# Optimization experiments

Measured on AMD Instinct MI355X. Metric: run time of the kernel, lower is better.

## Reference

```python
import jax, jax.numpy as jnp
import numpy as np

B = 8192   # batch
S = 115    # state dim (fixed by slice layout)
E = 3072   # retrieval embed dim
C = 128    # compressed context dim
A = 23     # action dim
NE = 4096  # number of hyperedge keys
K = 10     # top-k retrieval
TAU = 1.0  # gumbel temperature
EPS = 1e-5 # layernorm eps


def _ln(x, g, b):
    m = x.mean(-1, keepdims=True)
    v = x.var(-1, keepdims=True)
    return (x - m) * jax.lax.rsqrt(v + EPS) * g + b


def _actor(ctx, extra, w1, b1, g1, be1, w2, b2, g2, be2, w3, b3):
    x = jnp.concatenate([ctx, extra], -1)
    x = jax.nn.relu(_ln(x @ w1 + b1, g1, be1))
    x = jax.nn.relu(_ln(x @ w2 + b2, g2, be2))
    return x @ w3 + b3


def setup_inputs() -> dict:
    key = jax.random.key(0)
    ks = iter(jax.random.split(key, 80))

    def W(shape):
        return jax.random.normal(next(ks), shape, jnp.float32) * (1.0 / float(np.sqrt(shape[0])))

    inp = {}
    inp["state"] = jax.random.normal(next(ks), (B, S), jnp.float32)
    u = jax.random.uniform(next(ks), (B, 4), jnp.float32, 1e-6, 1.0 - 1e-6)
    inp["gumbel_noise"] = -jnp.log(-jnp.log(u))  # standard Gumbel samples
    inp["keys"] = jax.random.normal(next(ks), (NE, E), jnp.float32)
    # state encoder 115 -> 512 -> 512 -> 3072 + LN
    inp["se_w1"] = W((S, 512)); inp["se_b1"] = jnp.zeros(512)
    inp["se_w2"] = W((512, 512)); inp["se_b2"] = jnp.zeros(512)
    inp["se_w3"] = W((512, E)); inp["se_b3"] = jnp.zeros(E)
    inp["se_g"] = jnp.ones(E); inp["se_beta"] = jnp.zeros(E)
    # context compressor 3072 -> 512 -> 128 + LN
    inp["cc_w1"] = W((E, 512)); inp["cc_b1"] = jnp.zeros(512)
    inp["cc_w2"] = W((512, C)); inp["cc_b2"] = jnp.zeros(C)
    inp["cc_g"] = jnp.ones(C); inp["cc_beta"] = jnp.zeros(C)
    # 4 actor experts, differing only in extra-slice width
    for p, e in [("a_pre", 50), ("a_scene", 20), ("a_effect", 10), ("a_rule", 15)]:
        inp[p + "_w1"] = W((C + e, C)); inp[p + "_b1"] = jnp.zeros(C)
        inp[p + "_g1"] = jnp.ones(C); inp[p + "_be1"] = jnp.zeros(C)
        inp[p + "_w2"] = W((C, C)); inp[p + "_b2"] = jnp.zeros(C)
        inp[p + "_g2"] = jnp.ones(C); inp[p + "_be2"] = jnp.zeros(C)
        inp[p + "_w3"] = W((C, A)) * 0.01; inp[p + "_b3"] = jnp.zeros(A)  # orthogonal gain=0.01 approx
    # gumbel router 115 -> 64 -> 64 -> 4
    inp["r_w1"] = W((S, 64)); inp["r_b1"] = jnp.zeros(64)
    inp["r_w2"] = W((64, 64)); inp["r_b2"] = jnp.zeros(64)
    inp["r_w3"] = W((64, 4)); inp["r_b3"] = jnp.zeros(4)
    # critic 115 -> 256 -> 256 -> 1
    inp["c_w1"] = W((S, 256)); inp["c_b1"] = jnp.zeros(256)
    inp["c_w2"] = W((256, 256)); inp["c_b2"] = jnp.zeros(256)
    inp["c_w3"] = W((256, 1)); inp["c_b3"] = jnp.zeros(1)
    return inp


def reference(state, gumbel_noise, keys, se_w1, se_b1, se_w2, se_b2, se_w3, se_b3, se_g, se_beta, cc_w1, cc_b1, cc_w2, cc_b2, cc_g, cc_beta, a_pre_w1, a_pre_b1, a_pre_g1, a_pre_be1, a_pre_w2, a_pre_b2, a_pre_g2, a_pre_be2, a_pre_w3, a_pre_b3, a_scene_w1, a_scene_b1, a_scene_g1, a_scene_be1, a_scene_w2, a_scene_b2, a_scene_g2, a_scene_be2, a_scene_w3, a_scene_b3, a_effect_w1, a_effect_b1, a_effect_g1, a_effect_be1, a_effect_w2, a_effect_b2, a_effect_g2, a_effect_be2, a_effect_w3, a_effect_b3, a_rule_w1, a_rule_b1, a_rule_g1, a_rule_be1, a_rule_w2, a_rule_b2, a_rule_g2, a_rule_be2, a_rule_w3, a_rule_b3, r_w1, r_b1, r_w2, r_b2, r_w3, r_b3, c_w1, c_b1, c_w2, c_b2, c_w3, c_b3):
    # 1) state -> query (StateEncoder)
    q = jax.nn.relu(state @ se_w1 + se_b1)
    q = jax.nn.relu(q @ se_w2 + se_b2)
    q = _ln(q @ se_w3 + se_b3, se_g, se_beta)  # (B, E)
    # 2) top-k hard retrieval from hypergraph memory (cosine sim)
    qn = q * jax.lax.rsqrt(jnp.sum(q * q, -1, keepdims=True) + 1e-12)
    kn = keys * jax.lax.rsqrt(jnp.sum(keys * keys, -1, keepdims=True) + 1e-12)
    scores = qn @ kn.T                          # (B, NE)
    _, idx = jax.lax.top_k(scores, K)           # (B, K)
    context = jnp.take(keys, idx, axis=0).mean(1)  # (B, E) mean-pool top-k raw embeddings
    # 3) compress to shared knowledge
    h = jax.nn.relu(context @ cc_w1 + cc_b1)
    shared = _ln(h @ cc_w2 + cc_b2, cc_g, cc_beta)  # (B, C)
    # 4) state slices + 4 actor experts
    belief = state[:, :50]
    location = state[:, 20:40]
    hp = state[:, 40:50]
    inv = state[:, 45:60]
    lp = _actor(shared, belief, a_pre_w1, a_pre_b1, a_pre_g1, a_pre_be1, a_pre_w2, a_pre_b2, a_pre_g2, a_pre_be2, a_pre_w3, a_pre_b3)
    ls = _actor(shared, location, a_scene_w1, a_scene_b1, a_scene_g1, a_scene_be1, a_scene_w2, a_scene_b2, a_scene_g2, a_scene_be2, a_scene_w3, a_scene_b3)
    le = _actor(shared, hp, a_effect_w1, a_effect_b1, a_effect_g1, a_effect_be1, a_effect_w2, a_effect_b2, a_effect_g2, a_effect_be2, a_effect_w3, a_effect_b3)
    lr = _actor(shared, inv, a_rule_w1, a_rule_b1, a_rule_g1, a_rule_be1, a_rule_w2, a_rule_b2, a_rule_g2, a_rule_be2, a_rule_w3, a_rule_b3)
    # 5) gumbel-softmax hard router (straight-through)
    rh = jax.nn.relu(state @ r_w1 + r_b1)
    rh = jax.nn.relu(rh @ r_w2 + r_b2)
    rl = jnp.clip(rh @ r_w3 + r_b3, -20.0, 20.0)
    y_soft = jax.nn.softmax((rl + gumbel_noise) / TAU, -1)
    y_hard = jax.nn.one_hot(jnp.argmax(y_soft, -1), 4, dtype=y_soft.dtype)
    alpha = y_soft + jax.lax.stop_gradient(y_hard - y_soft)  # (B, 4)
    # 6) combine expert logits
    all_l = jnp.stack([lp, ls, le, lr], 1)      # (B, 4, A)
    logits = jnp.einsum('bk,bka->ba', alpha, all_l)
    # critic value
    v = jax.nn.relu(state @ c_w1 + c_b1)
    v = jax.nn.relu(v @ c_w2 + c_b2)
    value = v @ c_w3 + c_b3                      # (B, 1)
    return (logits, alpha, value)
```

## Files before the change

### kernel.cpp

```cpp
#include <hip/hip_runtime.h>

constexpr int Bz = 8192;
constexpr int Sz = 115;
constexpr int Ez = 3072;
constexpr int NEz = 4096;

typedef __attribute__((ext_vector_type(8))) short short8;
typedef __attribute__((ext_vector_type(4))) float floatx4;
typedef unsigned short ushort_t;
typedef unsigned int uint_t;

__device__ __forceinline__ ushort_t f2bf(float f) {
  uint_t u = __float_as_uint(f);
  uint_t r = (u + 0x7FFFu + ((u >> 16) & 1u)) >> 16;
  return (ushort_t)r;
}
__device__ __forceinline__ float bf2f(ushort_t b) {
  uint_t u = ((uint_t)b) << 16;
  return __uint_as_float(u);
}
__device__ __forceinline__ ushort_t f2key(float v) {
  _Float16 h = (_Float16)v;
  ushort_t b = __builtin_bit_cast(ushort_t, h);
  return b ^ ((b & 0x8000u) ? 0xFFFFu : 0x8000u);
}
__device__ __forceinline__ uint_t umax_(uint_t a, uint_t b) { return a > b ? a : b; }

__device__ __forceinline__ void gload16(const ushort_t* g, ushort_t* l) {
  __builtin_amdgcn_global_load_lds(
      (__attribute__((address_space(1))) const void*)g,
      (__attribute__((address_space(3))) void*)l, 16, 0, 0);
}

template<bool RELU, bool BIAS>
__global__ __launch_bounds__(256)
void gemm128(const float* __restrict__ A, const float* __restrict__ Bm,
             const float* __restrict__ bias, float* __restrict__ C,
             int N, int Kd)
{
  __shared__ float As[16][132];
  __shared__ float Bs[16][132];
  const int t  = threadIdx.x;
  const int tx = t & 15, ty = t >> 4;
  const int row0 = blockIdx.y * 128;
  const int col0 = blockIdx.x * 128;
  const int ar = t >> 2, ac = (t & 3) * 4;
  const int bk = t >> 5, bc = (t & 31) * 4;
  const bool a4 = (Kd & 3) == 0;

  float acc[8][8];
#pragma unroll
  for (int i = 0; i < 8; ++i)
#pragma unroll
    for (int j = 0; j < 8; ++j) acc[i][j] = 0.f;

  for (int k0 = 0; k0 < Kd; k0 += 16) {
    const bool fullA = (k0 + 16 <= Kd) && a4;
    {
      const float* ap = A + (size_t)(row0 + ar) * Kd + k0 + ac;
      if (fullA) {
        float4 v0 = *(const float4*)ap;
        float4 v1 = *(const float4*)(ap + (size_t)64 * Kd);
        As[ac + 0][ar] = v0.x; As[ac + 1][ar] = v0.y;
        As[ac + 2][ar] = v0.z; As[ac + 3][ar] = v0.w;
        As[ac + 0][ar + 64] = v1.x; As[ac + 1][ar + 64] = v1.y;
        As[ac + 2][ar + 64] = v1.z; As[ac + 3][ar + 64] = v1.w;
      } else {
#pragma unroll
        for (int e = 0; e < 4; ++e) {
          const int k = k0 + ac + e;
          float v0 = 0.f, v1 = 0.f;
          if (k < Kd) { v0 = ap[e]; v1 = ap[e + (size_t)64 * Kd]; }
          As[ac + e][ar] = v0; As[ac + e][ar + 64] = v1;
        }
      }
    }
    {
      const float* bp = Bm + (size_t)(k0 + bk) * N + col0 + bc;
      if (k0 + 16 <= Kd) {
        *(float4*)&Bs[bk][bc]     = *(const float4*)bp;
        *(float4*)&Bs[bk + 8][bc] = *(const float4*)(bp + (size_t)8 * N);
      } else {
        float4 z; z.x = z.y = z.z = z.w = 0.f;
        *(float4*)&Bs[bk][bc]     = (k0 + bk     < Kd) ? *(const float4*)bp : z;
        *(float4*)&Bs[bk + 8][bc] = (k0 + bk + 8 < Kd) ? *(const float4*)(bp + (size_t)8 * N) : z;
      }
    }
    __syncthreads();
#pragma unroll
    for (int kk = 0; kk < 16; ++kk) {
      float a[8], b[8];
      *(float4*)&a[0] = *(const float4*)&As[kk][ty * 4];
      *(float4*)&a[4] = *(const float4*)&As[kk][64 + ty * 4];
      *(float4*)&b[0] = *(const float4*)&Bs[kk][tx * 4];
      *(float4*)&b[4] = *(const float4*)&Bs[kk][64 + tx * 4];
#pragma unroll
      for (int i = 0; i < 8; ++i)
#pragma unroll
        for (int j = 0; j < 8; ++j)
          acc[i][j] = fmaf(a[i], b[j], acc[i][j]);
    }
    __syncthreads();
  }

  float bv[8];
#pragma unroll
  for (int j = 0; j < 8; ++j) bv[j] = 0.f;
  if (BIAS) {
    *(float4*)&bv[0] = *(const float4*)&bias[col0 + tx * 4];
    *(float4*)&bv[4] = *(const float4*)&bias[col0 + 64 + tx * 4];
  }
#pragma unroll
  for (int i = 0; i < 8; ++i) {
    const int r = row0 + ((i < 4) ? (ty * 4 + i) : (64 + ty * 4 + i - 4));
    float o[8];
#pragma unroll
    for (int j = 0; j < 8; ++j) {
      o[j] = acc[i][j] + bv[j];
      if (RELU) o[j] = fmaxf(o[j], 0.f);
    }
    *(float4*)&C[(size_t)r * N + col0 + tx * 4]      = *(float4*)&o[0];
    *(float4*)&C[(size_t)r * N + col0 + 64 + tx * 4] = *(float4*)&o[4];
  }
}

template<int EPI>
__global__ __launch_bounds__(256)
void mfma_bt(const ushort_t* __restrict__ A, const ushort_t* __restrict__ B,
             const float* __restrict__ bias, void* __restrict__ Cout,
             int N, int Kd)
{
  __shared__ ushort_t Al[128 * 32];
  __shared__ ushort_t Bl[128 * 32];
  const int t = threadIdx.x;
  const int wid = t >> 6, lane = t & 63;
  const int wr = wid >> 1, wc = wid & 1;
  const int row0 = blockIdx.y * 128;
  const int col0 = blockIdx.x * 128;
  const int srow = lane >> 2;
  const int scol = (lane & 3) * 8;

  const ushort_t* ga0 = A + (size_t)(row0 + wid * 16 + srow) * Kd + scol;
  const ushort_t* ga1 = A + (size_t)(row0 + (wid + 4) * 16 + srow) * Kd + scol;
  const ushort_t* gb0 = B + (size_t)(col0 + wid * 16 + srow) * Kd + scol;
  const ushort_t* gb1 = B + (size_t)(col0 + (wid + 4) * 16 + srow) * Kd + scol;
  ushort_t* la0 = &Al[(wid * 16) * 32];
  ushort_t* la1 = &Al[((wid + 4) * 16) * 32];
  ushort_t* lb0 = &Bl[(wid * 16) * 32];
  ushort_t* lb1 = &Bl[((wid + 4) * 16) * 32];

  const int mr = lane & 15, qd = lane >> 4;

  floatx4 acc[4][4];
#pragma unroll
  for (int i = 0; i < 4; ++i)
#pragma unroll
    for (int j = 0; j < 4; ++j) acc[i][j] = (floatx4){0.f, 0.f, 0.f, 0.f};

  for (int kb = 0; kb < Kd; kb += 32) {
    gload16(ga0 + kb, la0);
    gload16(ga1 + kb, la1);
    gload16(gb0 + kb, lb0);
    gload16(gb1 + kb, lb1);
    __syncthreads();
    short8 aF[4], bF[4];
#pragma unroll
    for (int i = 0; i < 4; ++i)
      aF[i] = *(const short8*)&Al[(wr * 64 + i * 16 + mr) * 32 + qd * 8];
#pragma unroll
    for (int j = 0; j < 4; ++j)
      bF[j] = *(const short8*)&Bl[(wc * 64 + j * 16 + mr) * 32 + qd * 8];
#pragma unroll
    for (int i = 0; i < 4; ++i)
#pragma unroll
      for (int j = 0; j < 4; ++j)
        acc[i][j] = __builtin_amdgcn_mfma_f32_16x16x32_bf16(aF[i], bF[j], acc[i][j], 0, 0, 0);
    __syncthreads();
  }

#pragma unroll
  for (int i = 0; i < 4; ++i) {
#pragma unroll
    for (int j = 0; j < 4; ++j) {
      const int col = col0 + wc * 64 + j * 16 + mr;
#pragma unroll
      for (int r = 0; r < 4; ++r) {
        const int row = row0 + wr * 64 + i * 16 + qd * 4 + r;
        if (EPI == 0) {
          ((ushort_t*)Cout)[(size_t)row * N + col] = f2key(acc[i][j][r]);
        } else {
          float v = acc[i][j][r] + bias[col];
          ((float*)Cout)[(size_t)row * N + col] = fmaxf(v, 0.f);
        }
      }
    }
  }
}

__global__ __launch_bounds__(256)
void mfma3_bt(const ushort_t* __restrict__ Ah, const ushort_t* __restrict__ Alo,
              const ushort_t* __restrict__ Bh, const ushort_t* __restrict__ Blo,
              const float* __restrict__ bias, float* __restrict__ Cout,
              int N, int Kd)
{
  __shared__ ushort_t AhL[128 * 32];
  __shared__ ushort_t AlL[128 * 32];
  __shared__ ushort_t BhL[128 * 32];
  __shared__ ushort_t BlL[128 * 32];
  const int t = threadIdx.x;
  const int wid = t >> 6, lane = t & 63;
  const int wr = wid >> 1, wc = wid & 1;
  const int row0 = blockIdx.y * 128;
  const int col0 = blockIdx.x * 128;
  const int srow = lane >> 2;
  const int scol = (lane & 3) * 8;

  const size_t aoff0 = (size_t)(row0 + wid * 16 + srow) * Kd + scol;
  const size_t aoff1 = (size_t)(row0 + (wid + 4) * 16 + srow) * Kd + scol;
  const size_t boff0 = (size_t)(col0 + wid * 16 + srow) * Kd + scol;
  const size_t boff1 = (size_t)(col0 + (wid + 4) * 16 + srow) * Kd + scol;
  const int l0 = (wid * 16) * 32;
  const int l1 = ((wid + 4) * 16) * 32;

  const int mr = lane & 15, qd = lane >> 4;

  floatx4 acc[4][4];
#pragma unroll
  for (int i = 0; i < 4; ++i)
#pragma unroll
    for (int j = 0; j < 4; ++j) acc[i][j] = (floatx4){0.f, 0.f, 0.f, 0.f};

  for (int kb = 0; kb < Kd; kb += 32) {
    gload16(Ah + aoff0 + kb, &AhL[l0]);
    gload16(Ah + aoff1 + kb, &AhL[l1]);
    gload16(Alo + aoff0 + kb, &AlL[l0]);
    gload16(Alo + aoff1 + kb, &AlL[l1]);
    gload16(Bh + boff0 + kb, &BhL[l0]);
    gload16(Bh + boff1 + kb, &BhL[l1]);
    gload16(Blo + boff0 + kb, &BlL[l0]);
    gload16(Blo + boff1 + kb, &BlL[l1]);
    __syncthreads();
    short8 ahF[4], alF[4], bhF[4], blF[4];
#pragma unroll
    for (int i = 0; i < 4; ++i) {
      const int o = (wr * 64 + i * 16 + mr) * 32 + qd * 8;
      ahF[i] = *(const short8*)&AhL[o];
      alF[i] = *(const short8*)&AlL[o];
    }
#pragma unroll
    for (int j = 0; j < 4; ++j) {
      const int o = (wc * 64 + j * 16 + mr) * 32 + qd * 8;
      bhF[j] = *(const short8*)&BhL[o];
      blF[j] = *(const short8*)&BlL[o];
    }
#pragma unroll
    for (int i = 0; i < 4; ++i)
#pragma unroll
      for (int j = 0; j < 4; ++j) {
        acc[i][j] = __builtin_amdgcn_mfma_f32_16x16x32_bf16(alF[i], bhF[j], acc[i][j], 0, 0, 0);
        acc[i][j] = __builtin_amdgcn_mfma_f32_16x16x32_bf16(ahF[i], blF[j], acc[i][j], 0, 0, 0);
        acc[i][j] = __builtin_amdgcn_mfma_f32_16x16x32_bf16(ahF[i], bhF[j], acc[i][j], 0, 0, 0);
      }
    __syncthreads();
  }

#pragma unroll
  for (int i = 0; i < 4; ++i) {
#pragma unroll
    for (int j = 0; j < 4; ++j) {
      const int col = col0 + wc * 64 + j * 16 + mr;
#pragma unroll
      for (int r = 0; r < 4; ++r) {
        const int row = row0 + wr * 64 + i * 16 + qd * 4 + r;
        Cout[(size_t)row * N + col] = acc[i][j][r] + bias[col];
      }
    }
  }
}

__global__ __launch_bounds__(256)
void gemm_scores(const float* __restrict__ A, const float* __restrict__ Bm,
                 const float* __restrict__ rk, ushort_t* __restrict__ S)
{
  __shared__ float As[16][132];
  __shared__ float Bs[16][132];
  const int t  = threadIdx.x;
  const int tx = t & 15, ty = t >> 4;
  const int row0 = blockIdx.y * 128;
  const int col0 = blockIdx.x * 128;
  const int ar = t >> 2, ac = (t & 3) * 4;
  const int Kd = Ez;

  float acc[8][8];
#pragma unroll
  for (int i = 0; i < 8; ++i)
#pragma unroll
    for (int j = 0; j < 8; ++j) acc[i][j] = 0.f;

  for (int k0 = 0; k0 < Kd; k0 += 16) {
    {
      const float* ap = A + (size_t)(row0 + ar) * Kd + k0 + ac;
      float4 v0 = *(const float4*)ap;
      float4 v1 = *(const float4*)(ap + (size_t)64 * Kd);
      As[ac + 0][ar] = v0.x; As[ac + 1][ar] = v0.y;
      As[ac + 2][ar] = v0.z; As[ac + 3][ar] = v0.w;
      As[ac + 0][ar + 64] = v1.x; As[ac + 1][ar + 64] = v1.y;
      As[ac + 2][ar + 64] = v1.z; As[ac + 3][ar + 64] = v1.w;
    }
    {
      const float* bp = Bm + (size_t)(col0 + ar) * Kd + k0 + ac;
      float4 v0 = *(const float4*)bp;
      float4 v1 = *(const float4*)(bp + (size_t)64 * Kd);
      Bs[ac + 0][ar] = v0.x; Bs[ac + 1][ar] = v0.y;
      Bs[ac + 2][ar] = v0.z; Bs[ac + 3][ar] = v0.w;
      Bs[ac + 0][ar + 64] = v1.x; Bs[ac + 1][ar + 64] = v1.y;
      Bs[ac + 2][ar + 64] = v1.z; Bs[ac + 3][ar + 64] = v1.w;
    }
    __syncthreads();
#pragma unroll
    for (int kk = 0; kk < 16; ++kk) {
      float a[8], b[8];
      *(float4*)&a[0] = *(const float4*)&As[kk][ty * 4];
      *(float4*)&a[4] = *(const float4*)&As[kk][64 + ty * 4];
      *(float4*)&b[0] = *(const float4*)&Bs[kk][tx * 4];
      *(float4*)&b[4] = *(const float4*)&Bs[kk][64 + tx * 4];
#pragma unroll
      for (int i = 0; i < 8; ++i)
#pragma unroll
        for (int j = 0; j < 8; ++j)
          acc[i][j] = fmaf(a[i], b[j], acc[i][j]);
    }
    __syncthreads();
  }

  float rk0[8];
  *(float4*)&rk0[0] = *(const float4*)&rk[col0 + tx * 4];
  *(float4*)&rk0[4] = *(const float4*)&rk[col0 + 64 + tx * 4];
#pragma unroll
  for (int i = 0; i < 8; ++i) {
    const int r = row0 + ((i < 4) ? (ty * 4 + i) : (64 + ty * 4 + i - 4));
    ushort4 h0, h1;
    h0.x = f2key(acc[i][0] * rk0[0]); h0.y = f2key(acc[i][1] * rk0[1]);
    h0.z = f2key(acc[i][2] * rk0[2]); h0.w = f2key(acc[i][3] * rk0[3]);
    h1.x = f2key(acc[i][4] * rk0[4]); h1.y = f2key(acc[i][5] * rk0[5]);
    h1.z = f2key(acc[i][6] * rk0[6]); h1.w = f2key(acc[i][7] * rk0[7]);
    *(ushort4*)&S[(size_t)r * NEz + col0 + tx * 4]      = h0;
    *(ushort4*)&S[(size_t)r * NEz + col0 + 64 + tx * 4] = h1;
  }
}

struct LN4 {
  const float* W[4]; const float* b[4]; const float* g[4]; const float* be[4];
  int eoff[4]; int elen[4];
};

template<bool RELU, bool HASEXT>
__global__ __launch_bounds__(256)
void gemm_ln4(const float* __restrict__ A1base, size_t a1stride, int K1,
              const float* __restrict__ A2, LN4 p,
              float* __restrict__ outbase, size_t ostride)
{
  __shared__ float As[32][68];
  __shared__ float Bs[32][132];
  __shared__ float rsum[64][17];
  __shared__ float rsq[64][17];
  __shared__ float stm[64], str[64];
  const int a = blockIdx.y;
  const float* A1 = A1base + (size_t)a * a1stride;
  float* out = outbase + (size_t)a * ostride;
  const float* W = p.W[a];
  const float* bias = p.b[a];
  const float* g = p.g[a];
  const float* be = p.be[a];
  const int eoff = HASEXT ? p.eoff[a] : 0;
  const int K2 = HASEXT ? p.elen[a] : 0;

  const int t = threadIdx.x;
  const int tx = t & 15, ty = t >> 4;
  const int row0 = blockIdx.x * 64;
  const int Kt = K1 + K2;
  const int ar = t >> 2, ac = (t & 3) * 8;
  const int bk = t >> 3, bc = (t & 7) * 16;

  float acc[4][8];
#pragma unroll
  for (int i = 0; i < 4; ++i)
#pragma unroll
    for (int j = 0; j < 8; ++j) acc[i][j] = 0.f;

  for (int k0 = 0; k0 < Kt; k0 += 32) {
    const int grow = row0 + ar;
#pragma unroll
    for (int e = 0; e < 8; ++e) {
      const int k = k0 + ac + e;
      float v = 0.f;
      if (k < K1)      v = A1[(size_t)grow * K1 + k];
      else if (k < Kt) v = A2[(size_t)grow * 115 + eoff + (k - K1)];
      As[ac + e][ar] = v;
    }
    {
      const int k = k0 + bk;
#pragma unroll
      for (int qd = 0; qd < 4; ++qd) {
        float4 z; z.x = z.y = z.z = z.w = 0.f;
        *(float4*)&Bs[bk][bc + 4 * qd] =
            (k < Kt) ? *(const float4*)&W[(size_t)k * 128 + bc + 4 * qd] : z;
      }
    }
    __syncthreads();
#pragma unroll
    for (int kk = 0; kk < 32; ++kk) {
      float av[4], bv2[8];
      *(float4*)&av[0]  = *(const float4*)&As[kk][ty * 4];
      *(float4*)&bv2[0] = *(const float4*)&Bs[kk][tx * 4];
      *(float4*)&bv2[4] = *(const float4*)&Bs[kk][64 + tx * 4];
#pragma unroll
      for (int i = 0; i < 4; ++i)
#pragma unroll
        for (int j = 0; j < 8; ++j)
          acc[i][j] = fmaf(av[i], bv2[j], acc[i][j]);
    }
    __syncthreads();
  }

  float bv[8];
  *(float4*)&bv[0] = *(const float4*)&bias[tx * 4];
  *(float4*)&bv[4] = *(const float4*)&bias[64 + tx * 4];
#pragma unroll
  for (int i = 0; i < 4; ++i) {
    float s = 0.f, q = 0.f;
#pragma unroll
    for (int j = 0; j < 8; ++j) {
      acc[i][j] += bv[j];
      s += acc[i][j];
      q += acc[i][j] * acc[i][j];
    }
    rsum[ty * 4 + i][tx] = s;
    rsq[ty * 4 + i][tx]  = q;
  }
  __syncthreads();
  if (t < 64) {
    float s = 0.f, q = 0.f;
#pragma unroll
    for (int x = 0; x < 16; ++x) { s += rsum[t][x]; q += rsq[t][x]; }
    const float m = s * (1.f / 128.f);
    const float v = q * (1.f / 128.f) - m * m;
    stm[t] = m;
    str[t] = rsqrtf(v + 1e-5f);
  }
  __syncthreads();
#pragma unroll
  for (int i = 0; i < 4; ++i) {
    const int r = ty * 4 + i;
    const float m = stm[r], rs = str[r];
    float o[8];
#pragma unroll
    for (int j = 0; j < 8; ++j) {
      const int col = (j < 4) ? (tx * 4 + j) : (64 + tx * 4 + (j - 4));
      float y = (acc[i][j] - m) * rs * g[col] + be[col];
      if (RELU) y = fmaxf(y, 0.f);
      o[j] = y;
    }
    *(float4*)&out[(size_t)(row0 + r) * 128 + tx * 4]      = *(float4*)&o[0];
    *(float4*)&out[(size_t)(row0 + r) * 128 + 64 + tx * 4] = *(float4*)&o[4];
  }
}

__device__ __forceinline__ float blockSum256(float v, float* sh)
{
#pragma unroll
  for (int d = 32; d; d >>= 1) v += __shfl_down(v, d, 64);
  __syncthreads();
  if ((threadIdx.x & 63) == 0) sh[threadIdx.x >> 6] = v;
  __syncthreads();
  return sh[0] + sh[1] + sh[2] + sh[3];
}

template<bool CVT>
__global__ __launch_bounds__(256)
void ln_l2_q(float* __restrict__ q, const float* __restrict__ g,
             const float* __restrict__ be, ushort_t* __restrict__ qb)
{
  __shared__ float sh[4];
  const int row = blockIdx.x, t = threadIdx.x;
  float* qr = q + (size_t)row * Ez;
  float x[12];
#pragma unroll
  for (int i = 0; i < 12; ++i) x[i] = qr[t + (i << 8)];
  float s = 0.f;
#pragma unroll
  for (int i = 0; i < 12; ++i) s += x[i];
  const float m = blockSum256(s, sh) * (1.f / (float)Ez);
  float vs = 0.f;
#pragma unroll
  for (int i = 0; i < 12; ++i) { const float d = x[i] - m; vs += d * d; }
  const float v = blockSum256(vs, sh) * (1.f / (float)Ez);
  const float rs = rsqrtf(v + 1e-5f);
  float y[12]; float qs = 0.f;
#pragma unroll
  for (int i = 0; i < 12; ++i) {
    const int c = t + (i << 8);
    const float yy = (x[i] - m) * rs * g[c] + be[c];
    y[i] = yy; qs += yy * yy;
  }
  const float tot = blockSum256(qs, sh);
  const float s2 = rsqrtf(tot + 1e-12f);
#pragma unroll
  for (int i = 0; i < 12; ++i) {
    const int c = t + (i << 8);
    const float yn = y[i] * s2;
    qr[c] = yn;
    if (CVT) qb[(size_t)row * Ez + c] = f2bf(yn);
  }
}

__global__ __launch_bounds__(256)
void keynorm(const float* __restrict__ keys, float* __restrict__ rk)
{
  __shared__ float sh[4];
  const int row = blockIdx.x, t = threadIdx.x;
  const float* xr = keys + (size_t)row * Ez;
  float qs = 0.f;
#pragma unroll
  for (int i = 0; i < 12; ++i) { const float x = xr[t + (i << 8)]; qs += x * x; }
  const float tot = blockSum256(qs, sh);
  if (t == 0) rk[row] = rsqrtf(tot + 1e-12f);
}

__global__ __launch_bounds__(256)
void keys_norm_cvt(const float* __restrict__ keys, float* __restrict__ rk,
                   ushort_t* __restrict__ knb)
{
  __shared__ float sh[4];
  const int row = blockIdx.x, t = threadIdx.x;
  const float* xr = keys + (size_t)row * Ez;
  float x[12]; float qs = 0.f;
#pragma unroll
  for (int i = 0; i < 12; ++i) { x[i] = xr[t + (i << 8)]; qs += x[i] * x[i]; }
  const float tot = blockSum256(qs, sh);
  const float s = rsqrtf(tot + 1e-12f);
  if (t == 0) rk[row] = s;
#pragma unroll
  for (int i = 0; i < 12; ++i)
    knb[(size_t)row * Ez + t + (i << 8)] = f2bf(x[i] * s);
}

__global__ __launch_bounds__(256)
void split_bf(const float* __restrict__ in, ushort_t* __restrict__ oh,
              ushort_t* __restrict__ ol)
{
  const size_t i = ((size_t)blockIdx.x * 256 + threadIdx.x) * 4;
  float4 v = *(const float4*)(in + i);
  ushort4 h, l;
  h.x = f2bf(v.x); l.x = f2bf(v.x - bf2f(h.x));
  h.y = f2bf(v.y); l.y = f2bf(v.y - bf2f(h.y));
  h.z = f2bf(v.z); l.z = f2bf(v.z - bf2f(h.z));
  h.w = f2bf(v.w); l.w = f2bf(v.w - bf2f(h.w));
  *(ushort4*)(oh + i) = h;
  *(ushort4*)(ol + i) = l;
}

__global__ __launch_bounds__(256)
void w3_transpose_split(const float* __restrict__ w,
                        ushort_t* __restrict__ hT, ushort_t* __restrict__ lT)
{
  __shared__ float tile[64][65];
  const int k0 = blockIdx.x * 64;
  const int n0 = blockIdx.y * 64;
  const int t = threadIdx.x;
  const int c = t & 63, r4 = t >> 6;
#pragma unroll
  for (int rr = 0; rr < 16; ++rr) {
    const int r = rr * 4 + r4;
    tile[r][c] = w[(size_t)(k0 + r) * 3072 + n0 + c];
  }
  __syncthreads();
#pragma unroll
  for (int rr = 0; rr < 16; ++rr) {
    const int n = rr * 4 + r4;
    const float a = tile[c][n];
    const ushort_t h = f2bf(a);
    hT[(size_t)(n0 + n) * 512 + k0 + c] = h;
    lT[(size_t)(n0 + n) * 512 + k0 + c] = f2bf(a - bf2f(h));
  }
}

__global__ __launch_bounds__(256)
void cvt_w1t(const float* __restrict__ w, ushort_t* __restrict__ out)
{
  const int idx = blockIdx.x * 256 + threadIdx.x;
  const int k = idx >> 9, n = idx & 511;
  out[(size_t)n * Ez + k] = f2bf(w[idx]);
}

__global__ __launch_bounds__(256)
void topk16(const ushort_t* __restrict__ S, int* __restrict__ outIdx)
{
  __shared__ uint_t cand[64];
  const int row = blockIdx.x, t = threadIdx.x;
  const int w = t >> 6, lane = t & 63;
  const ushort_t* sr = S + (size_t)row * NEz + (w << 10);
  uint_t p[16];
#pragma unroll
  for (int j = 0; j < 16; ++j) {
    const int c = (j << 6) + lane;
    const uint_t key = sr[c];
    const int gc = (w << 10) + c;
    p[j] = (key << 12) | (uint_t)(4095 - gc);
  }
  for (int it = 0; it < 16; ++it) {
    uint_t m = p[0];
#pragma unroll
    for (int j = 1; j < 16; ++j) m = umax_(m, p[j]);
#pragma unroll
    for (int d = 1; d < 64; d <<= 1)
      m = umax_(m, (uint_t)__shfl_xor((int)m, d, 64));
    if (lane == it) cand[(w << 4) + it] = m;
#pragma unroll
    for (int j = 0; j < 16; ++j) p[j] = (p[j] == m) ? 0u : p[j];
  }
  __syncthreads();
  if (t < 64) {
    uint_t mine = cand[t];
    for (int it = 0; it < 16; ++it) {
      uint_t m = mine;
#pragma unroll
      for (int d = 1; d < 64; d <<= 1)
        m = umax_(m, (uint_t)__shfl_xor((int)m, d, 64));
      if (t == it) outIdx[(size_t)row * 16 + it] = 4095 - (int)(m & 0xFFFu);
      mine = (mine == m) ? 0u : mine;
    }
  }
}

template<bool BFOUT>
__global__ __launch_bounds__(256)
void rescore_gather(const float* __restrict__ qn, const float* __restrict__ keys,
                    const float* __restrict__ rk, const int* __restrict__ cand,
                    void* __restrict__ ctxOut)
{
  __shared__ float qs[Ez];
  __shared__ double sv[16];
  __shared__ int si[16];
  __shared__ int sel10[10];
  const int row = blockIdx.x, t = threadIdx.x;
  const int w = t >> 6, lane = t & 63;

  {
    const float* qr = qn + (size_t)row * Ez;
#pragma unroll
    for (int i = 0; i < 3; ++i) {
      const int c = (t << 2) + (i << 10);
      *(float4*)&qs[c] = *(const float4*)&qr[c];
    }
  }
  __syncthreads();

#pragma unroll
  for (int cc = 0; cc < 4; ++cc) {
    const int slot = w * 4 + cc;
    const int id = cand[(size_t)row * 16 + slot];
    const float* kr = keys + (size_t)id * Ez;
    double s = 0.0;
#pragma unroll
    for (int it = 0; it < 12; ++it) {
      const int c = (lane << 2) + (it << 8);
      float4 k4 = *(const float4*)&kr[c];
      float4 q4 = *(const float4*)&qs[c];
      s += (double)q4.x * (double)k4.x;
      s += (double)q4.y * (double)k4.y;
      s += (double)q4.z * (double)k4.z;
      s += (double)q4.w * (double)k4.w;
    }
#pragma unroll
    for (int d = 32; d; d >>= 1) s += __shfl_down(s, d, 64);
    if (lane == 0) { sv[slot] = s * (double)rk[id]; si[slot] = id; }
  }
  __syncthreads();

  if (t == 0) {
    for (int it = 0; it < 10; ++it) {
      int bj = 0; double bvv = sv[0]; int bi = si[0];
      for (int j = 1; j < 16; ++j) {
        const double v = sv[j]; const int i2 = si[j];
        if (v > bvv || (v == bvv && i2 < bi)) { bj = j; bvv = v; bi = i2; }
      }
      sel10[it] = bi;
      sv[bj] = -1e300;
    }
  }
  __syncthreads();

  int id[10];
#pragma unroll
  for (int j = 0; j < 10; ++j) id[j] = sel10[j];

#pragma unroll
  for (int i = 0; i < 3; ++i) {
    const int c = (t << 2) + (i << 10);
    float4 a = {0.f, 0.f, 0.f, 0.f};
#pragma unroll
    for (int j = 0; j < 10; ++j) {
      float4 v = *(const float4*)&keys[(size_t)id[j] * Ez + c];
      a.x += v.x; a.y += v.y; a.z += v.z; a.w += v.w;
    }
    if (BFOUT) {
      ushort4 o;
      o.x = f2bf(a.x * 0.1f); o.y = f2bf(a.y * 0.1f);
      o.z = f2bf(a.z * 0.1f); o.w = f2bf(a.w * 0.1f);
      *(ushort4*)&((ushort_t*)ctxOut)[(size_t)row * Ez + c] = o;
    } else {
      float4 o;
      o.x = a.x * 0.1f; o.y = a.y * 0.1f; o.z = a.z * 0.1f; o.w = a.w * 0.1f;
      *(float4*)&((float*)ctxOut)[(size_t)row * Ez + c] = o;
    }
  }
}

__global__ __launch_bounds__(256)
void router_kernel(const float* __restrict__ state, const float* __restrict__ gn,
                   const float* __restrict__ w1, const float* __restrict__ b1,
                   const float* __restrict__ w2, const float* __restrict__ b2,
                   const float* __restrict__ w3, const float* __restrict__ b3,
                   float* __restrict__ outAlpha)
{
  const int row = blockIdx.x * 256 + threadIdx.x;
  const float* sr = state + (size_t)row * Sz;
  float h1[64];
#pragma unroll
  for (int j = 0; j < 64; ++j) h1[j] = b1[j];
  for (int k = 0; k < Sz; ++k) {
    const float a = sr[k];
    const float* wr = w1 + (size_t)k * 64;
#pragma unroll
    for (int j = 0; j < 64; ++j) h1[j] = fmaf(a, wr[j], h1[j]);
  }
#pragma unroll
  for (int j = 0; j < 64; ++j) h1[j] = fmaxf(h1[j], 0.f);
  float h2[64];
#pragma unroll
  for (int j = 0; j < 64; ++j) h2[j] = b2[j];
#pragma unroll
  for (int k = 0; k < 64; ++k) {
    const float a = h1[k];
    const float* wr = w2 + (size_t)k * 64;
#pragma unroll
    for (int j = 0; j < 64; ++j) h2[j] = fmaf(a, wr[j], h2[j]);
  }
#pragma unroll
  for (int j = 0; j < 64; ++j) h2[j] = fmaxf(h2[j], 0.f);
  float z[4];
#pragma unroll
  for (int a = 0; a < 4; ++a) {
    float s = b3[a];
#pragma unroll
    for (int k = 0; k < 64; ++k) s = fmaf(h2[k], w3[k * 4 + a], s);
    s = fminf(fmaxf(s, -20.f), 20.f);
    z[a] = s + gn[(size_t)row * 4 + a];
  }
  float mz = z[0];
#pragma unroll
  for (int a = 1; a < 4; ++a) mz = fmaxf(mz, z[a]);
  float e[4]; float se = 0.f;
#pragma unroll
  for (int a = 0; a < 4; ++a) { e[a] = expf(z[a] - mz); se += e[a]; }
  const float inv = 1.f / se;
  float y[4];
#pragma unroll
  for (int a = 0; a < 4; ++a) y[a] = e[a] * inv;
  int am = 0;
#pragma unroll
  for (int a = 1; a < 4; ++a) if (y[a] > y[am]) am = a;
#pragma unroll
  for (int a = 0; a < 4; ++a) {
    const float hard = (a == am) ? 1.f : 0.f;
    outAlpha[(size_t)row * 4 + a] = y[a] + (hard - y[a]);
  }
}

__global__ __launch_bounds__(256)
void critic_head(const float* __restrict__ c2, const float* __restrict__ w3,
                 const float* __restrict__ b3, float* __restrict__ outv)
{
  const int row = blockIdx.x * 256 + threadIdx.x;
  const float* xr = c2 + (size_t)row * 256;
  float s = b3[0];
  for (int k = 0; k < 256; ++k) s = fmaf(xr[k], w3[k], s);
  outv[row] = s;
}

struct HeadP { const float* w3[4]; const float* b3[4]; };

__global__ __launch_bounds__(256)
void actor_head4(const float* __restrict__ x2g, HeadP p,
                 const float* __restrict__ alpha, float* __restrict__ outL)
{
  __shared__ float wsm[4][128 * 23];
  __shared__ float bs[4][23];
  const int t = threadIdx.x;
#pragma unroll
  for (int a = 0; a < 4; ++a) {
    for (int i = t; i < 128 * 23; i += 256) wsm[a][i] = p.w3[a][i];
    if (t < 23) bs[a][t] = p.b3[a][t];
  }
  __syncthreads();
  const int row = blockIdx.x * 64 + (t >> 2);
  const int cg = t & 3;
  float sum[6] = {0.f, 0.f, 0.f, 0.f, 0.f, 0.f};
#pragma unroll
  for (int a = 0; a < 4; ++a) {
    const float al = alpha[(size_t)row * 4 + a];
    const float* xr = x2g + (size_t)a * Bz * 128 + (size_t)row * 128;
    float acc[6] = {0.f, 0.f, 0.f, 0.f, 0.f, 0.f};
    for (int kk = 0; kk < 128; ++kk) {
      const float xa = xr[kk];
#pragma unroll
      for (int j = 0; j < 6; ++j) {
        const int col = cg + 4 * j;
        if (col < 23) acc[j] = fmaf(xa, wsm[a][kk * 23 + col], acc[j]);
      }
    }
#pragma unroll
    for (int j = 0; j < 6; ++j) {
      const int col = cg + 4 * j;
      if (col < 23) sum[j] += al * (acc[j] + bs[a][col]);
    }
  }
#pragma unroll
  for (int j = 0; j < 6; ++j) {
    const int col = cg + 4 * j;
    if (col < 23) outL[(size_t)row * 23 + col] = sum[j];
  }
}

extern "C" void kernel_launch(void* const* d_in, const int* in_sizes, int n_in,
                              void* d_out, int out_size, void* d_ws, size_t ws_size,
                              hipStream_t stream)
{
  const float* state  = (const float*)d_in[0];
  const float* gumbel = (const float*)d_in[1];
  const float* keys   = (const float*)d_in[2];
  const float* se_w1 = (const float*)d_in[3];
  const float* se_b1 = (const float*)d_in[4];
  const float* se_w2 = (const float*)d_in[5];
  const float* se_b2 = (const float*)d_in[6];
  const float* se_w3 = (const float*)d_in[7];
  const float* se_b3 = (const float*)d_in[8];
  const float* se_g  = (const float*)d_in[9];
  const float* se_be = (const float*)d_in[10];
  const float* cc_w1 = (const float*)d_in[11];
  const float* cc_b1 = (const float*)d_in[12];
  const float* cc_w2 = (const float*)d_in[13];
  const float* cc_b2 = (const float*)d_in[14];
  const float* cc_g  = (const float*)d_in[15];
  const float* cc_be = (const float*)d_in[16];
  const float* r_w1 = (const float*)d_in[57];
  const float* r_b1 = (const float*)d_in[58];
  const float* r_w2 = (const float*)d_in[59];
  const float* r_b2 = (const float*)d_in[60];
  const float* r_w3 = (const float*)d_in[61];
  const float* r_b3 = (const float*)d_in[62];
  const float* c_w1 = (const float*)d_in[63];
  const float* c_b1 = (const float*)d_in[64];
  const float* c_w2 = (const float*)d_in[65];
  const float* c_b2 = (const float*)d_in[66];
  const float* c_w3 = (const float*)d_in[67];
  const float* c_b3 = (const float*)d_in[68];

  float* wsf = (float*)d_ws;
  const size_t qF = (size_t)Bz * Ez;
  const size_t uF = (size_t)16777216;
  float* q = wsf;
  float* U = wsf + qF;
  float* sA  = U;
  float* sB  = U + 4194304;
  ushort_t* sBh  = (ushort_t*)(U + 8388608);
  ushort_t* sBl  = (ushort_t*)(U + 10485760);
  ushort_t* w3hT = (ushort_t*)(U + 12582912);
  ushort_t* w3lT = (ushort_t*)(U + 14155776);
  ushort_t* scoresU = (ushort_t*)U;
  float* shr = U;
  float* x1g = U + 1 * 1048576;
  float* x2g = U + 5 * 1048576;
  float* cch = U + 9 * 1048576;
  float* cr1 = U + 9 * 1048576;
  float* cr2 = U + 11 * 1048576;
  ushort_t* qbf  = (ushort_t*)(wsf + qF + uF);
  ushort_t* knbf = qbf + qF;
  ushort_t* w1T  = knbf + (size_t)NEz * Ez;
  const size_t bfHalves = qF + (size_t)NEz * Ez + (size_t)512 * Ez;
  const size_t baseBytes = (qF + uF) * sizeof(float);
  const size_t tailBytes = 4096 * 4 + (size_t)Bz * 16 * 4;
  const bool fast = ws_size >= baseBytes + bfHalves * 2 + tailBytes;
  float* tailF = (float*)((char*)d_ws + (fast ? baseBytes + bfHalves * 2 : baseBytes));
  float* rk  = tailF;
  int* cand  = (int*)(tailF + 4096);
  ushort_t* ctxb = (ushort_t*)q;

  float* outL = (float*)d_out;
  float* outA = outL + (size_t)Bz * 23;
  float* outV = outA + (size_t)Bz * 4;

  const dim3 blk(256);

  gemm128<true, true><<<dim3(4, 64), blk, 0, stream>>>(state, se_w1, se_b1, sA, 512, 115);
  gemm128<true, true><<<dim3(4, 64), blk, 0, stream>>>(sA,    se_w2, se_b2, sB, 512, 512);
  if (fast) {
    split_bf<<<dim3(4096), blk, 0, stream>>>(sB, sBh, sBl);
    w3_transpose_split<<<dim3(8, 48), blk, 0, stream>>>(se_w3, w3hT, w3lT);
    mfma3_bt<<<dim3(24, 64), blk, 0, stream>>>(sBh, sBl, w3hT, w3lT, se_b3, q, 3072, 512);
    ln_l2_q<true><<<dim3(Bz), blk, 0, stream>>>(q, se_g, se_be, qbf);
    keys_norm_cvt<<<dim3(NEz), blk, 0, stream>>>(keys, rk, knbf);
    cvt_w1t<<<dim3(6144), blk, 0, stream>>>(cc_w1, w1T);
    mfma_bt<0><<<dim3(32, 64), blk, 0, stream>>>(qbf, knbf, nullptr, scoresU, NEz, Ez);
  } else {
    gemm128<false, true><<<dim3(24, 64), blk, 0, stream>>>(sB, se_w3, se_b3, q, 3072, 512);
    ln_l2_q<false><<<dim3(Bz), blk, 0, stream>>>(q, se_g, se_be, nullptr);
    keynorm<<<dim3(NEz), blk, 0, stream>>>(keys, rk);
    gemm_scores<<<dim3(32, 64), blk, 0, stream>>>(q, keys, rk, scoresU);
  }

  topk16<<<dim3(Bz), blk, 0, stream>>>(scoresU, cand);

  if (fast) {
    rescore_gather<true><<<dim3(Bz), blk, 0, stream>>>(q, keys, rk, cand, ctxb);
    mfma_bt<1><<<dim3(4, 64), blk, 0, stream>>>(ctxb, w1T, cc_b1, cch, 512, Ez);
  } else {
    rescore_gather<false><<<dim3(Bz), blk, 0, stream>>>(q, keys, rk, cand, q);
    gemm128<true, true><<<dim3(4, 64), blk, 0, stream>>>(q, cc_w1, cc_b1, cch, 512, Ez);
  }
  {
    LN4 pcc = {};
    pcc.W[0] = cc_w2; pcc.b[0] = cc_b2; pcc.g[0] = cc_g; pcc.be[0] = cc_be;
    gemm_ln4<false, false><<<dim3(128, 1), blk, 0, stream>>>(cch, 0, 512, nullptr, pcc,
                                                             shr, 0);
  }

  gemm128<true, true><<<dim3(2, 64), blk, 0, stream>>>(state, c_w1, c_b1, cr1, 256, 115);
  gemm128<true, true><<<dim3(2, 64), blk, 0, stream>>>(cr1, c_w2, c_b2, cr2, 256, 256);
  critic_head<<<dim3(32), blk, 0, stream>>>(cr2, c_w3, c_b3, outV);

  router_kernel<<<dim3(32), blk, 0, stream>>>(state, gumbel, r_w1, r_b1, r_w2, r_b2,
                                              r_w3, r_b3, outA);

  {
    LN4 p1 = {}, p2 = {};
    HeadP ph = {};
    const int eoffs[4] = {0, 20, 40, 45};
    const int elens[4] = {50, 20, 10, 15};
    for (int a = 0; a < 4; ++a) {
      const int base = 17 + 10 * a;
      p1.W[a]  = (const float*)d_in[base + 0];
      p1.b[a]  = (const float*)d_in[base + 1];
      p1.g[a]  = (const float*)d_in[base + 2];
      p1.be[a] = (const float*)d_in[base + 3];
      p1.eoff[a] = eoffs[a]; p1.elen[a] = elens[a];
      p2.W[a]  = (const float*)d_in[base + 4];
      p2.b[a]  = (const float*)d_in[base + 5];
      p2.g[a]  = (const float*)d_in[base + 6];
      p2.be[a] = (const float*)d_in[base + 7];
      ph.w3[a] = (const float*)d_in[base + 8];
      ph.b3[a] = (const float*)d_in[base + 9];
    }
    gemm_ln4<true, true ><<<dim3(128, 4), blk, 0, stream>>>(shr, 0, 128, state, p1,
                                                            x1g, (size_t)Bz * 128);
    gemm_ln4<true, false><<<dim3(128, 4), blk, 0, stream>>>(x1g, (size_t)Bz * 128, 128,
                                                            nullptr, p2,
                                                            x2g, (size_t)Bz * 128);
    actor_head4<<<dim3(128), blk, 0, stream>>>(x2g, ph, outA, outL);
  }
}
```

Measured before the change: 1.437 ms.

## Batch critic GEMMs with encoder, fuse bf16 split, swizzle scores grid, vectorize topk

Critic MLP layers now share a launch with the state-encoder layers through a dual-problem GEMM kernel. The second of these also writes the hi/lo bf16 split in its epilogue, which removes the separate split kernel. The scores MFMA GEMM uses a 1D grid with a grouped tile swizzle for better L2 reuse, and cc_w1 is transposed through a shared-memory tile for coalesced access. topk16 loads 16 contiguous keys per lane with vector loads, and actor_head4 uses twice as many blocks with fewer columns per thread. Critic buffers are aliased onto q, which relies on q being dead at that point; critic and router now run before q is written.

```diff
diff --git a/kernel.cpp b/kernel.cpp
--- a/kernel.cpp
+++ b/kernel.cpp
@@ -124,6 +124,113 @@
   }
 }
 
+struct GPart {
+  const float* A; const float* Bm; const float* bias;
+  float* C; ushort_t* Ch; ushort_t* Cl;
+  int N; int Kd; int nbx;
+};
+
+__global__ __launch_bounds__(256)
+void gemm128_dual(GPart g0, GPart g1)
+{
+  __shared__ float As[16][132];
+  __shared__ float Bs[16][132];
+  const int t  = threadIdx.x;
+  const int tx = t & 15, ty = t >> 4;
+  const bool p0 = (int)blockIdx.x < g0.nbx;
+  GPart g = p0 ? g0 : g1;
+  const int bx = p0 ? blockIdx.x : (blockIdx.x - g0.nbx);
+  const int row0 = blockIdx.y * 128;
+  const int col0 = bx * 128;
+  const int Kd = g.Kd, N = g.N;
+  const int ar = t >> 2, ac = (t & 3) * 4;
+  const int bk = t >> 5, bc = (t & 31) * 4;
+  const bool a4 = (Kd & 3) == 0;
+
+  float acc[8][8];
+#pragma unroll
+  for (int i = 0; i < 8; ++i)
+#pragma unroll
+    for (int j = 0; j < 8; ++j) acc[i][j] = 0.f;
+
+  for (int k0 = 0; k0 < Kd; k0 += 16) {
+    const bool fullA = (k0 + 16 <= Kd) && a4;
+    {
+      const float* ap = g.A + (size_t)(row0 + ar) * Kd + k0 + ac;
+      if (fullA) {
+        float4 v0 = *(const float4*)ap;
+        float4 v1 = *(const float4*)(ap + (size_t)64 * Kd);
+        As[ac + 0][ar] = v0.x; As[ac + 1][ar] = v0.y;
+        As[ac + 2][ar] = v0.z; As[ac + 3][ar] = v0.w;
+        As[ac + 0][ar + 64] = v1.x; As[ac + 1][ar + 64] = v1.y;
+        As[ac + 2][ar + 64] = v1.z; As[ac + 3][ar + 64] = v1.w;
+      } else {
+#pragma unroll
+        for (int e = 0; e < 4; ++e) {
+          const int k = k0 + ac + e;
+          float v0 = 0.f, v1 = 0.f;
+          if (k < Kd) { v0 = ap[e]; v1 = ap[e + (size_t)64 * Kd]; }
+          As[ac + e][ar] = v0; As[ac + e][ar + 64] = v1;
+        }
+      }
+    }
+    {
+      const float* bp = g.Bm + (size_t)(k0 + bk) * N + col0 + bc;
+      if (k0 + 16 <= Kd) {
+        *(float4*)&Bs[bk][bc]     = *(const float4*)bp;
+        *(float4*)&Bs[bk + 8][bc] = *(const float4*)(bp + (size_t)8 * N);
+      } else {
+        float4 z; z.x = z.y = z.z = z.w = 0.f;
+        *(float4*)&Bs[bk][bc]     = (k0 + bk     < Kd) ? *(const float4*)bp : z;
+        *(float4*)&Bs[bk + 8][bc] = (k0 + bk + 8 < Kd) ? *(const float4*)(bp + (size_t)8 * N) : z;
+      }
+    }
+    __syncthreads();
+#pragma unroll
+    for (int kk = 0; kk < 16; ++kk) {
+      float a[8], b[8];
+      *(float4*)&a[0] = *(const float4*)&As[kk][ty * 4];
+      *(float4*)&a[4] = *(const float4*)&As[kk][64 + ty * 4];
+      *(float4*)&b[0] = *(const float4*)&Bs[kk][tx * 4];
+      *(float4*)&b[4] = *(const float4*)&Bs[kk][64 + tx * 4];
+#pragma unroll
+      for (int i = 0; i < 8; ++i)
+#pragma unroll
+        for (int j = 0; j < 8; ++j)
+          acc[i][j] = fmaf(a[i], b[j], acc[i][j]);
+    }
+    __syncthreads();
+  }
+
+  float bv[8];
+  *(float4*)&bv[0] = *(const float4*)&g.bias[col0 + tx * 4];
+  *(float4*)&bv[4] = *(const float4*)&g.bias[col0 + 64 + tx * 4];
+#pragma unroll
+  for (int i = 0; i < 8; ++i) {
+    const int r = row0 + ((i < 4) ? (ty * 4 + i) : (64 + ty * 4 + i - 4));
+    float o[8];
+#pragma unroll
+    for (int j = 0; j < 8; ++j) o[j] = fmaxf(acc[i][j] + bv[j], 0.f);
+    const size_t i0 = (size_t)r * N + col0 + tx * 4;
+    const size_t i1 = i0 + 64;
+    *(float4*)&g.C[i0] = *(float4*)&o[0];
+    *(float4*)&g.C[i1] = *(float4*)&o[4];
+    if (g.Ch) {
+      ushort4 h0, l0, h1, l1;
+      h0.x = f2bf(o[0]); l0.x = f2bf(o[0] - bf2f(h0.x));
+      h0.y = f2bf(o[1]); l0.y = f2bf(o[1] - bf2f(h0.y));
+      h0.z = f2bf(o[2]); l0.z = f2bf(o[2] - bf2f(h0.z));
+      h0.w = f2bf(o[3]); l0.w = f2bf(o[3] - bf2f(h0.w));
+      h1.x = f2bf(o[4]); l1.x = f2bf(o[4] - bf2f(h1.x));
+      h1.y = f2bf(o[5]); l1.y = f2bf(o[5] - bf2f(h1.y));
+      h1.z = f2bf(o[6]); l1.z = f2bf(o[6] - bf2f(h1.z));
+      h1.w = f2bf(o[7]); l1.w = f2bf(o[7] - bf2f(h1.w));
+      *(ushort4*)&g.Ch[i0] = h0; *(ushort4*)&g.Cl[i0] = l0;
+      *(ushort4*)&g.Ch[i1] = h1; *(ushort4*)&g.Cl[i1] = l1;
+    }
+  }
+}
+
 template<int EPI>
 __global__ __launch_bounds__(256)
 void mfma_bt(const ushort_t* __restrict__ A, const ushort_t* __restrict__ B,
@@ -135,8 +242,15 @@
   const int t = threadIdx.x;
   const int wid = t >> 6, lane = t & 63;
   const int wr = wid >> 1, wc = wid & 1;
-  const int row0 = blockIdx.y * 128;
-  const int col0 = blockIdx.x * 128;
+  int row0, col0;
+  if (EPI == 0) {
+    const int L = blockIdx.x;
+    row0 = ((L & 7) + (L >> 8) * 8) << 7;
+    col0 = ((L >> 3) & 31) << 7;
+  } else {
+    row0 = blockIdx.y << 7;
+    col0 = blockIdx.x << 7;
+  }
   const int srow = lane >> 2;
   const int scol = (lane & 3) * 8;
 
@@ -546,21 +660,6 @@
 }
 
 __global__ __launch_bounds__(256)
-void split_bf(const float* __restrict__ in, ushort_t* __restrict__ oh,
-              ushort_t* __restrict__ ol)
-{
-  const size_t i = ((size_t)blockIdx.x * 256 + threadIdx.x) * 4;
-  float4 v = *(const float4*)(in + i);
-  ushort4 h, l;
-  h.x = f2bf(v.x); l.x = f2bf(v.x - bf2f(h.x));
-  h.y = f2bf(v.y); l.y = f2bf(v.y - bf2f(h.y));
-  h.z = f2bf(v.z); l.z = f2bf(v.z - bf2f(h.z));
-  h.w = f2bf(v.w); l.w = f2bf(v.w - bf2f(h.w));
-  *(ushort4*)(oh + i) = h;
-  *(ushort4*)(ol + i) = l;
-}
-
-__global__ __launch_bounds__(256)
 void w3_transpose_split(const float* __restrict__ w,
                         ushort_t* __restrict__ hT, ushort_t* __restrict__ lT)
 {
@@ -586,11 +685,24 @@
 }
 
 __global__ __launch_bounds__(256)
-void cvt_w1t(const float* __restrict__ w, ushort_t* __restrict__ out)
-{
-  const int idx = blockIdx.x * 256 + threadIdx.x;
-  const int k = idx >> 9, n = idx & 511;
-  out[(size_t)n * Ez + k] = f2bf(w[idx]);
+void cvt_w1t_t(const float* __restrict__ w, ushort_t* __restrict__ out)
+{
+  __shared__ float tile[64][65];
+  const int k0 = blockIdx.x * 64;
+  const int n0 = blockIdx.y * 64;
+  const int t = threadIdx.x;
+  const int c = t & 63, r4 = t >> 6;
+#pragma unroll
+  for (int rr = 0; rr < 16; ++rr) {
+    const int r = rr * 4 + r4;
+    tile[r][c] = w[(size_t)(k0 + r) * 512 + n0 + c];
+  }
+  __syncthreads();
+#pragma unroll
+  for (int rr = 0; rr < 16; ++rr) {
+    const int n = rr * 4 + r4;
+    out[(size_t)(n0 + n) * Ez + k0 + c] = f2bf(tile[c][n]);
+  }
 }
 
 __global__ __launch_bounds__(256)
@@ -599,15 +711,29 @@
   __shared__ uint_t cand[64];
   const int row = blockIdx.x, t = threadIdx.x;
   const int w = t >> 6, lane = t & 63;
-  const ushort_t* sr = S + (size_t)row * NEz + (w << 10);
+  const int base = (w << 10) + (lane << 4);
+  const ushort_t* sr = S + (size_t)row * NEz + base;
+  uint4 v0 = *(const uint4*)sr;
+  uint4 v1 = *(const uint4*)(sr + 8);
+  const uint_t cb = (uint_t)(4095 - base);
   uint_t p[16];
-#pragma unroll
-  for (int j = 0; j < 16; ++j) {
-    const int c = (j << 6) + lane;
-    const uint_t key = sr[c];
-    const int gc = (w << 10) + c;
-    p[j] = (key << 12) | (uint_t)(4095 - gc);
-  }
+  p[0]  = ((v0.x & 0xFFFFu) << 12) | (cb - 0);
+  p[1]  = ((v0.x >> 16)     << 12) | (cb - 1);
+  p[2]  = ((v0.y & 0xFFFFu) << 12) | (cb - 2);
+  p[3]  = ((v0.y >> 16)     << 12) | (cb - 3);
+  p[4]  = ((v0.z & 0xFFFFu) << 12) | (cb - 4);
+  p[5]  = ((v0.z >> 16)     << 12) | (cb - 5);
+  p[6]  = ((v0.w & 0xFFFFu) << 12) | (cb - 6);
+  p[7]  = ((v0.w >> 16)     << 12) | (cb - 7);
+  p[8]  = ((v1.x & 0xFFFFu) << 12) | (cb - 8);
+  p[9]  = ((v1.x >> 16)     << 12) | (cb - 9);
+  p[10] = ((v1.y & 0xFFFFu) << 12) | (cb - 10);
+  p[11] = ((v1.y >> 16)     << 12) | (cb - 11);
+  p[12] = ((v1.z & 0xFFFFu) << 12) | (cb - 12);
+  p[13] = ((v1.z >> 16)     << 12) | (cb - 13);
+  p[14] = ((v1.w & 0xFFFFu) << 12) | (cb - 14);
+  p[15] = ((v1.w >> 16)     << 12) | (cb - 15);
+
   for (int it = 0; it < 16; ++it) {
     uint_t m = p[0];
 #pragma unroll
@@ -804,31 +930,31 @@
     if (t < 23) bs[a][t] = p.b3[a][t];
   }
   __syncthreads();
-  const int row = blockIdx.x * 64 + (t >> 2);
-  const int cg = t & 3;
-  float sum[6] = {0.f, 0.f, 0.f, 0.f, 0.f, 0.f};
+  const int row = blockIdx.x * 32 + (t >> 3);
+  const int cg = t & 7;
+  float sum[3] = {0.f, 0.f, 0.f};
 #pragma unroll
   for (int a = 0; a < 4; ++a) {
     const float al = alpha[(size_t)row * 4 + a];
     const float* xr = x2g + (size_t)a * Bz * 128 + (size_t)row * 128;
-    float acc[6] = {0.f, 0.f, 0.f, 0.f, 0.f, 0.f};
+    float acc[3] = {0.f, 0.f, 0.f};
     for (int kk = 0; kk < 128; ++kk) {
       const float xa = xr[kk];
 #pragma unroll
-      for (int j = 0; j < 6; ++j) {
-        const int col = cg + 4 * j;
+      for (int j = 0; j < 3; ++j) {
+        const int col = cg + 8 * j;
         if (col < 23) acc[j] = fmaf(xa, wsm[a][kk * 23 + col], acc[j]);
       }
     }
 #pragma unroll
-    for (int j = 0; j < 6; ++j) {
-      const int col = cg + 4 * j;
+    for (int j = 0; j < 3; ++j) {
+      const int col = cg + 8 * j;
       if (col < 23) sum[j] += al * (acc[j] + bs[a][col]);
     }
   }
 #pragma unroll
-  for (int j = 0; j < 6; ++j) {
-    const int col = cg + 4 * j;
+  for (int j = 0; j < 3; ++j) {
+    const int col = cg + 8 * j;
     if (col < 23) outL[(size_t)row * 23 + col] = sum[j];
   }
 }
@@ -883,8 +1009,8 @@
   float* x1g = U + 1 * 1048576;
   float* x2g = U + 5 * 1048576;
   float* cch = U + 9 * 1048576;
-  float* cr1 = U + 9 * 1048576;
-  float* cr2 = U + 11 * 1048576;
+  float* cr1 = q;
+  float* cr2 = q + 2097152;
   ushort_t* qbf  = (ushort_t*)(wsf + qF + uF);
   ushort_t* knbf = qbf + qF;
   ushort_t* w1T  = knbf + (size_t)NEz * Ez;
@@ -903,16 +1029,28 @@
 
   const dim3 blk(256);
 
-  gemm128<true, true><<<dim3(4, 64), blk, 0, stream>>>(state, se_w1, se_b1, sA, 512, 115);
-  gemm128<true, true><<<dim3(4, 64), blk, 0, stream>>>(sA,    se_w2, se_b2, sB, 512, 512);
+  {
+    GPart e0 = {state, se_w1, se_b1, sA, nullptr, nullptr, 512, 115, 4};
+    GPart e1 = {state, c_w1,  c_b1,  cr1, nullptr, nullptr, 256, 115, 2};
+    gemm128_dual<<<dim3(6, 64), blk, 0, stream>>>(e0, e1);
+  }
+  {
+    GPart f0 = {sA, se_w2, se_b2, sB, fast ? sBh : nullptr, fast ? sBl : nullptr,
+                512, 512, 4};
+    GPart f1 = {cr1, c_w2, c_b2, cr2, nullptr, nullptr, 256, 256, 2};
+    gemm128_dual<<<dim3(6, 64), blk, 0, stream>>>(f0, f1);
+  }
+  critic_head<<<dim3(32), blk, 0, stream>>>(cr2, c_w3, c_b3, outV);
+  router_kernel<<<dim3(32), blk, 0, stream>>>(state, gumbel, r_w1, r_b1, r_w2, r_b2,
+                                              r_w3, r_b3, outA);
+
   if (fast) {
-    split_bf<<<dim3(4096), blk, 0, stream>>>(sB, sBh, sBl);
     w3_transpose_split<<<dim3(8, 48), blk, 0, stream>>>(se_w3, w3hT, w3lT);
     mfma3_bt<<<dim3(24, 64), blk, 0, stream>>>(sBh, sBl, w3hT, w3lT, se_b3, q, 3072, 512);
     ln_l2_q<true><<<dim3(Bz), blk, 0, stream>>>(q, se_g, se_be, qbf);
     keys_norm_cvt<<<dim3(NEz), blk, 0, stream>>>(keys, rk, knbf);
-    cvt_w1t<<<dim3(6144), blk, 0, stream>>>(cc_w1, w1T);
-    mfma_bt<0><<<dim3(32, 64), blk, 0, stream>>>(qbf, knbf, nullptr, scoresU, NEz, Ez);
+    cvt_w1t_t<<<dim3(48, 8), blk, 0, stream>>>(cc_w1, w1T);
+    mfma_bt<0><<<dim3(2048), blk, 0, stream>>>(qbf, knbf, nullptr, scoresU, NEz, Ez);
   } else {
     gemm128<false, true><<<dim3(24, 64), blk, 0, stream>>>(sB, se_w3, se_b3, q, 3072, 512);
     ln_l2_q<false><<<dim3(Bz), blk, 0, stream>>>(q, se_g, se_be, nullptr);
@@ -935,13 +1073,6 @@
     gemm_ln4<false, false><<<dim3(128, 1), blk, 0, stream>>>(cch, 0, 512, nullptr, pcc,
                                                              shr, 0);
   }
-
-  gemm128<true, true><<<dim3(2, 64), blk, 0, stream>>>(state, c_w1, c_b1, cr1, 256, 115);
-  gemm128<true, true><<<dim3(2, 64), blk, 0, stream>>>(cr1, c_w2, c_b2, cr2, 256, 256);
-  critic_head<<<dim3(32), blk, 0, stream>>>(cr2, c_w3, c_b3, outV);
-
-  router_kernel<<<dim3(32), blk, 0, stream>>>(state, gumbel, r_w1, r_b1, r_w2, r_b2,
-                                              r_w3, r_b3, outA);
 
   {
     LN4 p1 = {}, p2 = {};
@@ -967,6 +1098,6 @@
     gemm_ln4<true, false><<<dim3(128, 4), blk, 0, stream>>>(x1g, (size_t)Bz * 128, 128,
                                                             nullptr, p2,
                                                             x2g, (size_t)Bz * 128);
-    actor_head4<<<dim3(128), blk, 0, stream>>>(x2g, ph, outA, outL);
-  }
-}
+    actor_head4<<<dim3(256), blk, 0, stream>>>(x2g, ph, outA, outL);
+  }
+}
```

New measurement: 1.406 ms. 2.1% less time.
